# Kernel tuning notes

Hardware: AMD Instinct MI355X
Metric: run time of the kernel (lower is better)

The kernel has to match this reference:

```python
import jax, jax.numpy as jnp
import numpy as np

UNITS = [100, 80, 50, 30]
D_IN = 64


def _lstm_layer(x, Wx, Wh, b):
    # x: [B, T, D]; Wx: [D, 4u]; Wh: [u, 4u]; b: [4u]
    B = x.shape[0]
    u = Wh.shape[0]
    # precompute input contribution for all timesteps: [B, T, 4u]
    xg = jnp.einsum('btd,dg->btg', x, Wx) + b

    def step(carry, xg_t):
        h, c = carry
        g = xg_t + h @ Wh                      # [B, 4u]
        i, f, cbar, o = jnp.split(g, 4, axis=-1)
        i = jax.nn.sigmoid(i)
        f = jax.nn.sigmoid(f)
        o = jax.nn.sigmoid(o)
        c = f * c + i * jnp.tanh(cbar)
        h = o * jnp.tanh(c)
        return (h, c), h

    init = (jnp.zeros((B, u), x.dtype), jnp.zeros((B, u), x.dtype))
    (h_final, _), hs = jax.lax.scan(step, init, jnp.swapaxes(xg, 0, 1))
    return jnp.swapaxes(hs, 0, 1), h_final  # [B, T, u], [B, u]


def setup_inputs() -> dict:
    key = jax.random.key(0)
    ks = jax.random.split(key, 16)
    B, T = 256, 1024
    inp = {"sequence": jax.random.normal(ks[0], (B, T, D_IN), dtype=jnp.float32)}
    d_in = D_IN
    for li, u in enumerate(UNITS):
        s_x = 1.0 / np.sqrt(d_in)
        s_h = 1.0 / np.sqrt(u)
        inp[f"Wx{li}"] = jax.random.normal(ks[1 + 3 * li], (d_in, 4 * u), dtype=jnp.float32) * s_x
        inp[f"Wh{li}"] = jax.random.normal(ks[2 + 3 * li], (u, 4 * u), dtype=jnp.float32) * s_h
        inp[f"b{li}"] = jnp.zeros((4 * u,), dtype=jnp.float32)
        d_in = u
    inp["W_out"] = jax.random.normal(ks[13], (UNITS[-1], 1), dtype=jnp.float32) / np.sqrt(UNITS[-1])
    inp["b_out"] = jnp.zeros((1,), dtype=jnp.float32)
    return inp


def reference(sequence, Wx0, Wh0, b0, Wx1, Wh1, b1, Wx2, Wh2, b2, Wx3, Wh3, b3, W_out, b_out):
    # 4 stacked LSTM layers; dropout is identity at inference.
    x, _ = _lstm_layer(sequence, Wx0, Wh0, b0)   # [B, T, 100]
    x, _ = _lstm_layer(x, Wx1, Wh1, b1)          # [B, T, 80]
    x, _ = _lstm_layer(x, Wx2, Wh2, b2)          # [B, T, 50]
    _, h = _lstm_layer(x, Wx3, Wh3, b3)          # final state [B, 30]
    return h @ W_out + b_out                     # [B, 1]
```

## Files before the change

### kernel.cpp

```cpp
#include <hip/hip_runtime.h>


#define BATCH 256
#define TFULL 1024
#define TC    64
#define NCHUNK (TFULL / TC)
#define NDIAG  (NCHUNK + 3)

typedef __attribute__((ext_vector_type(2))) _Float16 f16x2;
typedef __attribute__((ext_vector_type(4))) _Float16 f16x4;

__device__ __forceinline__ float fast_rcp(float x) {
    return __builtin_amdgcn_rcpf(x);
}

__device__ __forceinline__ float tanh_fast(float x) {
    float e = __expf(-2.0f * fabsf(x));
    float r = fast_rcp(1.0f + e);
    return copysignf(fmaf(2.0f, r, -1.0f), x);
}

__device__ __forceinline__ float fdot2_(f16x2 a, f16x2 b, float c) {
#if __has_builtin(__builtin_amdgcn_fdot2)
    return __builtin_amdgcn_fdot2(a, b, c, false);
#else
    float d;
    asm("v_dot2_f32_f16 %0, %1, %2, %3" : "=v"(d) : "v"(a), "v"(b), "v"(c));
    return d;
#endif
}

__device__ __forceinline__ void lds_barrier() {
    asm volatile("s_waitcnt lgkmcnt(0)\n\ts_barrier" ::: "memory");
}

template<int CTRL>
__device__ __forceinline__ float dpp_add(float v) {
    int t = __builtin_amdgcn_update_dpp(0, __float_as_int(v), CTRL, 0xF, 0xF, true);
    return v + __int_as_float(t);
}
template<int CTRL>
__device__ __forceinline__ float dpp_mov(float v) {
    int t = __builtin_amdgcn_update_dpp(0, __float_as_int(v), CTRL, 0xF, 0xF, true);
    return __int_as_float(t);
}

template<int K, int N>
__device__ __forceinline__ void gemm_body(
    const float* __restrict__ x, int batchStride,
    const float* __restrict__ Wx,
    const float* __restrict__ bias,
    float* __restrict__ out,
    int lid, float* __restrict__ smem)
{
    constexpr int K4   = (K + 3) / 4;
    constexpr int SLAB = 64 * 4 + 4;
    constexpr int GX   = (N + 63) / 64;

    float* s_A = smem;
    float* s_B = smem + K4 * SLAB;

    const int n0   = (lid % GX) * 64;
    const int row0 = (lid / GX) * 64;
    const int tid  = threadIdx.x;
    const int tx   = tid & 15;
    const int ty   = tid >> 4;

    if constexpr ((K % 4) == 0) {
        for (int i = tid; i < 64 * (K / 4); i += 256) {
            const int row = i / (K / 4);
            const int k4  = i % (K / 4);
            const int gr  = row0 + row;
            const int b   = gr >> 6;
            const int t   = gr & 63;
            float4 v = *(const float4*)(x + (size_t)b * batchStride + t * K + k4 * 4);
            *(float4*)(s_A + k4 * SLAB + row * 4) = v;
        }
    } else {
        for (int i = tid; i < 64 * K; i += 256) {
            const int row = i / K;
            const int k   = i % K;
            const int gr  = row0 + row;
            const int b   = gr >> 6;
            const int t   = gr & 63;
            s_A[(k >> 2) * SLAB + row * 4 + (k & 3)] =
                x[(size_t)b * batchStride + t * K + k];
        }
        constexpr int PAD = K4 * 4 - K;
        for (int i = tid; i < 64 * PAD; i += 256) {
            const int row = i / PAD;
            const int kk  = K + i % PAD;
            s_A[(kk >> 2) * SLAB + row * 4 + (kk & 3)] = 0.0f;
        }
    }

    for (int i = tid; i < K4 * 4 * 16; i += 256) {
        const int k  = i >> 4;
        const int c4 = i & 15;
        float4 v = {0.0f, 0.0f, 0.0f, 0.0f};
        if (k < K && n0 + c4 * 4 < N)
            v = *(const float4*)(Wx + (size_t)k * N + n0 + c4 * 4);
        *(float4*)(s_B + k * 64 + c4 * 4) = v;
    }
    __syncthreads();

    float acc[4][4];
#pragma unroll
    for (int r = 0; r < 4; ++r)
#pragma unroll
        for (int c = 0; c < 4; ++c) acc[r][c] = 0.0f;

    for (int k4 = 0; k4 < K4; ++k4) {
        float4 bv[4];
#pragma unroll
        for (int j = 0; j < 4; ++j)
            bv[j] = *(const float4*)(s_B + (k4 * 4 + j) * 64 + tx * 4);
#pragma unroll
        for (int r = 0; r < 4; ++r) {
            float4 av = *(const float4*)(s_A + k4 * SLAB + (ty + 16 * r) * 4);
#pragma unroll
            for (int c = 0; c < 4; ++c) {
                acc[r][c] = fmaf(av.x, ((const float*)&bv[0])[c], acc[r][c]);
                acc[r][c] = fmaf(av.y, ((const float*)&bv[1])[c], acc[r][c]);
                acc[r][c] = fmaf(av.z, ((const float*)&bv[2])[c], acc[r][c]);
                acc[r][c] = fmaf(av.w, ((const float*)&bv[3])[c], acc[r][c]);
            }
        }
    }

    if (n0 + tx * 4 < N) {
        float4 bb = *(const float4*)(bias + n0 + tx * 4);
#pragma unroll
        for (int r = 0; r < 4; ++r) {
            float4 o;
            o.x = acc[r][0] + bb.x;
            o.y = acc[r][1] + bb.y;
            o.z = acc[r][2] + bb.z;
            o.w = acc[r][3] + bb.w;
            *(float4*)(out + (size_t)(row0 + ty + 16 * r) * N + n0 + tx * 4) = o;
        }
    }
}

struct GemmArgs {
    const float *x0, *x1, *x2, *x3;
    float *o0, *o1, *o2, *o3;
    const float *Wx0, *bi0, *Wx1, *bi1, *Wx2, *bi2, *Wx3, *bi3;
    int off1, off2, off3;
};

__global__ __launch_bounds__(256, 2)
void xg_all(GemmArgs a)
{
    __shared__ __align__(16) float smem[12900];
    const int bid = blockIdx.x;
    if (bid < a.off1)
        gemm_body<64, 400>(a.x0, TFULL * 64, a.Wx0, a.bi0, a.o0, bid, smem);
    else if (bid < a.off2)
        gemm_body<100, 320>(a.x1, TC * 100, a.Wx1, a.bi1, a.o1, bid - a.off1, smem);
    else if (bid < a.off3)
        gemm_body<80, 200>(a.x2, TC * 80, a.Wx2, a.bi2, a.o2, bid - a.off2, smem);
    else
        gemm_body<50, 120>(a.x3, TC * 50, a.Wx3, a.bi3, a.o3, bid - a.off3, smem);
}

template<int U, int S, int BLOCK, bool LAST>
__device__ __forceinline__ void rec4_body(
    _Float16* __restrict__ s_h,
    const float* __restrict__ xg,
    const float* __restrict__ Wh,
    float* __restrict__ xout,
    float* __restrict__ c_state,
    float* __restrict__ h_state,
    int first, int b,
    const float* __restrict__ Wout,
    const float* __restrict__ bout,
    float* __restrict__ dout)
{
    constexpr int G  = 4 * U;
    constexpr int HS = 4 * S;

    const int tid = threadIdx.x;
    const int u   = tid >> 2;
    const int s   = tid & 3;
    const bool act_th = (u < U);
    const int uu  = act_th ? u : 0;
    const bool wave_act = ((tid & ~63) < 4 * U);

    f16x2 w4[4][S / 2];
#pragma unroll
    for (int g = 0; g < 4; ++g)
#pragma unroll
        for (int kk = 0; kk < S; kk += 2) {
            const int k0 = s * S + kk;
            const int k1 = k0 + 1;
            const float wa = (act_th && k0 < U) ? Wh[(size_t)k0 * G + g * U + uu] : 0.0f;
            const float wb = (act_th && k1 < U) ? Wh[(size_t)k1 * G + g * U + uu] : 0.0f;
            w4[g][kk >> 1] = (f16x2){(_Float16)wa, (_Float16)wb};
        }

    for (int i = tid; i < 2 * HS; i += BLOCK) s_h[i] = (_Float16)0.0f;
    __syncthreads();
    if (tid < U) s_h[tid] = (_Float16)(first ? 0.0f : h_state[b * U + tid]);
    float c = first ? 0.0f : c_state[b * U + uu];
    __syncthreads();

    const float* xgp = xg + (size_t)b * TC * G + (s * U + uu);
    float xg0 = xgp[0];
    float xg1 = xgp[G];

    int cur = 0;
    float h = 0.0f, hprev = 0.0f;
    const bool is_t = (s == 2);

    for (int t = 0; t < TC; ++t, cur ^= 1) {
        if (wave_act) {
            const int tp = (t + 2 < TC) ? (t + 2) : (TC - 1);
            const float xg2 = xgp[(size_t)tp * G];

            if (!LAST) {
                if (act_th && s == 0 && t > 0)
                    xout[((size_t)b * TC + (t - 1)) * U + u] = hprev;
            }

            float a0 = 0.0f, a1 = 0.0f, a2 = 0.0f, a3 = 0.0f;
            const _Float16* hs = s_h + cur * HS + s * S;
#pragma unroll
            for (int kk = 0; kk < S; kk += 4) {
                f16x4 v = *(const f16x4*)(hs + kk);
                f16x2 lo = __builtin_shufflevector(v, v, 0, 1);
                f16x2 hi = __builtin_shufflevector(v, v, 2, 3);
                const int p = kk >> 1;
                a0 = fdot2_(lo, w4[0][p],     a0);
                a0 = fdot2_(hi, w4[0][p + 1], a0);
                a1 = fdot2_(lo, w4[1][p],     a1);
                a1 = fdot2_(hi, w4[1][p + 1], a1);
                a2 = fdot2_(lo, w4[2][p],     a2);
                a2 = fdot2_(hi, w4[2][p + 1], a2);
                a3 = fdot2_(lo, w4[3][p],     a3);
                a3 = fdot2_(hi, w4[3][p + 1], a3);
            }

            a0 = dpp_add<0xB1>(a0); a0 = dpp_add<0x4E>(a0);
            a1 = dpp_add<0xB1>(a1); a1 = dpp_add<0x4E>(a1);
            a2 = dpp_add<0xB1>(a2); a2 = dpp_add<0x4E>(a2);
            a3 = dpp_add<0xB1>(a3); a3 = dpp_add<0x4E>(a3);

            const float asum = (s == 0) ? a0 : (s == 1) ? a1 : (s == 2) ? a2 : a3;
            const float gs = asum + xg0;
            const float y  = is_t ? (-2.0f * fabsf(gs)) : (-gs);
            const float r  = fast_rcp(1.0f + __expf(y));
            const float v  = is_t ? copysignf(fmaf(2.0f, r, -1.0f), gs) : r;

            const float fi = dpp_mov<0x00>(v);
            const float ff = dpp_mov<0x55>(v);
            const float tc = dpp_mov<0xAA>(v);
            const float fo = dpp_mov<0xFF>(v);
            c = fmaf(ff, c, fi * tc);
            h = fo * tanh_fast(c);

            const int nxt = cur ^ 1;
            if (act_th && s == 0) s_h[nxt * HS + u] = (_Float16)h;
            hprev = h;
            xg0 = xg1; xg1 = xg2;
        }
        lds_barrier();
    }

    if (!LAST) {
        if (act_th && s == 0)
            xout[((size_t)b * TC + (TC - 1)) * U + u] = hprev;
    }
    if (act_th && s == 0) {
        c_state[b * U + u] = c;
        h_state[b * U + u] = h;
    }
    if (LAST && tid == 0) {
        float acc = bout[0];
#pragma unroll
        for (int k = 0; k < U; ++k)
            acc = fmaf((float)s_h[cur * HS + k], Wout[k], acc);
        dout[b] = acc;
    }
}

struct RecArgs {
    const float *xg0, *xg1, *xg2, *xg3;
    const float *Wh0, *Wh1, *Wh2, *Wh3;
    float *xc0, *xc1, *xc2;
    float *c0, *h0, *c1, *h1, *c2, *h2, *c3, *h3;
    const float *Wout, *bout;
    float *dout;
    int d;
};

__global__ __attribute__((amdgpu_flat_work_group_size(448, 448),
                          amdgpu_waves_per_eu(4, 8)))
void rec_all(RecArgs a)
{
    __shared__ __align__(16) _Float16 s_h[2 * 112];
    const int grp = blockIdx.x >> 8;
    const int b   = blockIdx.x & 255;
    const int j   = a.d - grp;
    if (j < 0 || j >= NCHUNK) return;
    const int first = (j == 0) ? 1 : 0;
    switch (grp) {
    case 0: rec4_body<100, 28, 448, false>(s_h, a.xg0, a.Wh0, a.xc0, a.c0, a.h0,
                                           first, b, nullptr, nullptr, nullptr); break;
    case 1: rec4_body< 80, 20, 448, false>(s_h, a.xg1, a.Wh1, a.xc1, a.c1, a.h1,
                                           first, b, nullptr, nullptr, nullptr); break;
    case 2: rec4_body< 50, 16, 448, false>(s_h, a.xg2, a.Wh2, a.xc2, a.c2, a.h2,
                                           first, b, nullptr, nullptr, nullptr); break;
    default: rec4_body< 30,  8, 448, true >(s_h, a.xg3, a.Wh3, nullptr, a.c3, a.h3,
                                           first, b, a.Wout, a.bout, a.dout); break;
    }
}

extern "C" void kernel_launch(void* const* d_in, const int* in_sizes, int n_in,
                              void* d_out, int out_size, void* d_ws, size_t ws_size,
                              hipStream_t stream)
{
    const float* seq  = (const float*)d_in[0];
    const float* Wx0  = (const float*)d_in[1];
    const float* Wh0  = (const float*)d_in[2];
    const float* b0   = (const float*)d_in[3];
    const float* Wx1  = (const float*)d_in[4];
    const float* Wh1  = (const float*)d_in[5];
    const float* b1   = (const float*)d_in[6];
    const float* Wx2  = (const float*)d_in[7];
    const float* Wh2  = (const float*)d_in[8];
    const float* b2   = (const float*)d_in[9];
    const float* Wx3  = (const float*)d_in[10];
    const float* Wh3  = (const float*)d_in[11];
    const float* b3   = (const float*)d_in[12];
    const float* Wout = (const float*)d_in[13];
    const float* bout = (const float*)d_in[14];
    float* out = (float*)d_out;

    float* ws  = (float*)d_ws;
    float* XG0 = ws;
    float* XG1 = XG0 + (size_t)BATCH * TC * 400;
    float* XG2 = XG1 + (size_t)BATCH * TC * 320;
    float* XG3 = XG2 + (size_t)BATCH * TC * 200;
    float* XC0 = XG3 + (size_t)BATCH * TC * 120;
    float* XC1 = XC0 + (size_t)BATCH * TC * 100;
    float* XC2 = XC1 + (size_t)BATCH * TC * 80;
    float* st  = XC2 + (size_t)BATCH * TC * 50;
    float* sc0 = st + 0 * 32768; float* sh0 = st + 1 * 32768;
    float* sc1 = st + 2 * 32768; float* sh1 = st + 3 * 32768;
    float* sc2 = st + 4 * 32768; float* sh2 = st + 5 * 32768;
    float* sc3 = st + 6 * 32768; float* sh3 = st + 7 * 32768;

    const int NB0 = 7 * 256, NB1 = 5 * 256, NB2 = 4 * 256, NB3 = 2 * 256;

    for (int d = 0; d < NDIAG; ++d) {
        GemmArgs ga;
        ga.x0 = nullptr; ga.x1 = nullptr; ga.x2 = nullptr; ga.x3 = nullptr;
        ga.o0 = XG0; ga.o1 = XG1; ga.o2 = XG2; ga.o3 = XG3;
        ga.Wx0 = Wx0; ga.bi0 = b0; ga.Wx1 = Wx1; ga.bi1 = b1;
        ga.Wx2 = Wx2; ga.bi2 = b2; ga.Wx3 = Wx3; ga.bi3 = b3;
        int nb = 0;
        if (d < NCHUNK)                { ga.x0 = seq + (size_t)d * TC * 64; nb += NB0; }
        ga.off1 = nb;
        if (d >= 1 && d - 1 < NCHUNK)  { ga.x1 = XC0; nb += NB1; }
        ga.off2 = nb;
        if (d >= 2 && d - 2 < NCHUNK)  { ga.x2 = XC1; nb += NB2; }
        ga.off3 = nb;
        if (d >= 3 && d - 3 < NCHUNK)  { ga.x3 = XC2; nb += NB3; }

        xg_all<<<dim3(nb), dim3(256), 0, stream>>>(ga);

        RecArgs ra;
        ra.xg0 = XG0; ra.xg1 = XG1; ra.xg2 = XG2; ra.xg3 = XG3;
        ra.Wh0 = Wh0; ra.Wh1 = Wh1; ra.Wh2 = Wh2; ra.Wh3 = Wh3;
        ra.xc0 = XC0; ra.xc1 = XC1; ra.xc2 = XC2;
        ra.c0 = sc0; ra.h0 = sh0; ra.c1 = sc1; ra.h1 = sh1;
        ra.c2 = sc2; ra.h2 = sh2; ra.c3 = sc3; ra.h3 = sh3;
        ra.Wout = Wout; ra.bout = bout; ra.dout = out;
        ra.d = d;

        rec_all<<<dim3(4 * 256), dim3(448), 0, stream>>>(ra);
    }
}
```

Baseline: 3.086 ms.

## Split each hidden unit's recurrence across two lanes instead of four

Restructures the recurrent kernel so each hidden unit is handled by 2 lanes instead of 4. Each lane now computes half of the K-dimension dot product for all four gates and evaluates two gate nonlinearities. The block shrinks from 448 to 256 threads, and the reductions and gate exchanges need fewer DPP steps. In exchange, each lane does twice as many fdot2 operations and holds twice as many weight registers; waves_per_eu is pinned to 1.

```diff
diff --git a/kernel.cpp b/kernel.cpp
--- a/kernel.cpp
+++ b/kernel.cpp
@@ -165,7 +165,7 @@
 }
 
 template<int U, int S, int BLOCK, bool LAST>
-__device__ __forceinline__ void rec4_body(
+__device__ __forceinline__ void rec2_body(
     _Float16* __restrict__ s_h,
     const float* __restrict__ xg,
     const float* __restrict__ Wh,
@@ -178,25 +178,25 @@
     float* __restrict__ dout)
 {
     constexpr int G  = 4 * U;
-    constexpr int HS = 4 * S;
+    constexpr int HS = 2 * S;
 
     const int tid = threadIdx.x;
-    const int u   = tid >> 2;
-    const int s   = tid & 3;
+    const int u   = tid >> 1;
+    const int s   = tid & 1;
     const bool act_th = (u < U);
     const int uu  = act_th ? u : 0;
-    const bool wave_act = ((tid & ~63) < 4 * U);
-
-    f16x2 w4[4][S / 2];
+    const bool wave_act = ((tid & ~63) < 2 * U);
+
+    f16x2 w[4][S / 2];
 #pragma unroll
     for (int g = 0; g < 4; ++g)
 #pragma unroll
-        for (int kk = 0; kk < S; kk += 2) {
-            const int k0 = s * S + kk;
+        for (int p = 0; p < S / 2; ++p) {
+            const int k0 = s * S + 2 * p;
             const int k1 = k0 + 1;
             const float wa = (act_th && k0 < U) ? Wh[(size_t)k0 * G + g * U + uu] : 0.0f;
             const float wb = (act_th && k1 < U) ? Wh[(size_t)k1 * G + g * U + uu] : 0.0f;
-            w4[g][kk >> 1] = (f16x2){(_Float16)wa, (_Float16)wb};
+            w[g][p] = (f16x2){(_Float16)wa, (_Float16)wb};
         }
 
     for (int i = tid; i < 2 * HS; i += BLOCK) s_h[i] = (_Float16)0.0f;
@@ -205,18 +205,20 @@
     float c = first ? 0.0f : c_state[b * U + uu];
     __syncthreads();
 
-    const float* xgp = xg + (size_t)b * TC * G + (s * U + uu);
-    float xg0 = xgp[0];
-    float xg1 = xgp[G];
+    const float* xgpA = xg + (size_t)b * TC * G + (s * U + uu);
+    const float* xgpB = xgpA + 2 * U;
+    float xA0 = xgpA[0], xA1 = xgpA[G];
+    float xB0 = xgpB[0], xB1 = xgpB[G];
 
     int cur = 0;
     float h = 0.0f, hprev = 0.0f;
-    const bool is_t = (s == 2);
+    const bool is_t = (s == 0);
 
     for (int t = 0; t < TC; ++t, cur ^= 1) {
         if (wave_act) {
             const int tp = (t + 2 < TC) ? (t + 2) : (TC - 1);
-            const float xg2 = xgp[(size_t)tp * G];
+            const float xA2 = xgpA[(size_t)tp * G];
+            const float xB2 = xgpB[(size_t)tp * G];
 
             if (!LAST) {
                 if (act_th && s == 0 && t > 0)
@@ -231,38 +233,42 @@
                 f16x2 lo = __builtin_shufflevector(v, v, 0, 1);
                 f16x2 hi = __builtin_shufflevector(v, v, 2, 3);
                 const int p = kk >> 1;
-                a0 = fdot2_(lo, w4[0][p],     a0);
-                a0 = fdot2_(hi, w4[0][p + 1], a0);
-                a1 = fdot2_(lo, w4[1][p],     a1);
-                a1 = fdot2_(hi, w4[1][p + 1], a1);
-                a2 = fdot2_(lo, w4[2][p],     a2);
-                a2 = fdot2_(hi, w4[2][p + 1], a2);
-                a3 = fdot2_(lo, w4[3][p],     a3);
-                a3 = fdot2_(hi, w4[3][p + 1], a3);
+                a0 = fdot2_(lo, w[0][p],     a0);
+                a0 = fdot2_(hi, w[0][p + 1], a0);
+                a1 = fdot2_(lo, w[1][p],     a1);
+                a1 = fdot2_(hi, w[1][p + 1], a1);
+                a2 = fdot2_(lo, w[2][p],     a2);
+                a2 = fdot2_(hi, w[2][p + 1], a2);
+                a3 = fdot2_(lo, w[3][p],     a3);
+                a3 = fdot2_(hi, w[3][p + 1], a3);
             }
 
-            a0 = dpp_add<0xB1>(a0); a0 = dpp_add<0x4E>(a0);
-            a1 = dpp_add<0xB1>(a1); a1 = dpp_add<0x4E>(a1);
-            a2 = dpp_add<0xB1>(a2); a2 = dpp_add<0x4E>(a2);
-            a3 = dpp_add<0xB1>(a3); a3 = dpp_add<0x4E>(a3);
-
-            const float asum = (s == 0) ? a0 : (s == 1) ? a1 : (s == 2) ? a2 : a3;
-            const float gs = asum + xg0;
-            const float y  = is_t ? (-2.0f * fabsf(gs)) : (-gs);
-            const float r  = fast_rcp(1.0f + __expf(y));
-            const float v  = is_t ? copysignf(fmaf(2.0f, r, -1.0f), gs) : r;
-
-            const float fi = dpp_mov<0x00>(v);
-            const float ff = dpp_mov<0x55>(v);
-            const float tc = dpp_mov<0xAA>(v);
-            const float fo = dpp_mov<0xFF>(v);
+            a0 = dpp_add<0xB1>(a0);
+            a1 = dpp_add<0xB1>(a1);
+            a2 = dpp_add<0xB1>(a2);
+            a3 = dpp_add<0xB1>(a3);
+
+            const float gA = ((s == 0) ? a0 : a1) + xA0;
+            const float gB = ((s == 0) ? a2 : a3) + xB0;
+            const float rA = fast_rcp(1.0f + __expf(-gA));
+            const float yB = is_t ? (-2.0f * fabsf(gB)) : (-gB);
+            const float rB = fast_rcp(1.0f + __expf(yB));
+            const float vB = is_t ? copysignf(fmaf(2.0f, rB, -1.0f), gB) : rB;
+
+            const float Asw = dpp_mov<0xB1>(rA);
+            const float Bsw = dpp_mov<0xB1>(vB);
+            const float fi = (s == 0) ? rA  : Asw;
+            const float ff = (s == 0) ? Asw : rA;
+            const float tc = (s == 0) ? vB  : Bsw;
+            const float fo = (s == 0) ? Bsw : vB;
             c = fmaf(ff, c, fi * tc);
             h = fo * tanh_fast(c);
 
             const int nxt = cur ^ 1;
             if (act_th && s == 0) s_h[nxt * HS + u] = (_Float16)h;
             hprev = h;
-            xg0 = xg1; xg1 = xg2;
+            xA0 = xA1; xA1 = xA2;
+            xB0 = xB1; xB1 = xB2;
         }
         lds_barrier();
     }
@@ -294,24 +300,24 @@
     int d;
 };
 
-__global__ __attribute__((amdgpu_flat_work_group_size(448, 448),
-                          amdgpu_waves_per_eu(4, 8)))
+__global__ __attribute__((amdgpu_flat_work_group_size(256, 256),
+                          amdgpu_waves_per_eu(1, 1)))
 void rec_all(RecArgs a)
 {
-    __shared__ __align__(16) _Float16 s_h[2 * 112];
+    __shared__ __align__(16) _Float16 s_h[2 * 104];
     const int grp = blockIdx.x >> 8;
     const int b   = blockIdx.x & 255;
     const int j   = a.d - grp;
     if (j < 0 || j >= NCHUNK) return;
     const int first = (j == 0) ? 1 : 0;
     switch (grp) {
-    case 0: rec4_body<100, 28, 448, false>(s_h, a.xg0, a.Wh0, a.xc0, a.c0, a.h0,
+    case 0: rec2_body<100, 52, 256, false>(s_h, a.xg0, a.Wh0, a.xc0, a.c0, a.h0,
                                            first, b, nullptr, nullptr, nullptr); break;
-    case 1: rec4_body< 80, 20, 448, false>(s_h, a.xg1, a.Wh1, a.xc1, a.c1, a.h1,
+    case 1: rec2_body< 80, 40, 256, false>(s_h, a.xg1, a.Wh1, a.xc1, a.c1, a.h1,
                                            first, b, nullptr, nullptr, nullptr); break;
-    case 2: rec4_body< 50, 16, 448, false>(s_h, a.xg2, a.Wh2, a.xc2, a.c2, a.h2,
+    case 2: rec2_body< 50, 28, 256, false>(s_h, a.xg2, a.Wh2, a.xc2, a.c2, a.h2,
                                            first, b, nullptr, nullptr, nullptr); break;
-    default: rec4_body< 30,  8, 448, true >(s_h, a.xg3, a.Wh3, nullptr, a.c3, a.h3,
+    default: rec2_body< 30, 16, 256, true >(s_h, a.xg3, a.Wh3, nullptr, a.c3, a.h3,
                                            first, b, a.Wout, a.bout, a.dout); break;
     }
 }
@@ -379,6 +385,6 @@
         ra.Wout = Wout; ra.bout = bout; ra.dout = out;
         ra.d = d;
 
-        rec_all<<<dim3(4 * 256), dim3(448), 0, stream>>>(ra);
-    }
-}
+        rec_all<<<dim3(4 * 256), dim3(256), 0, stream>>>(ra);
+    }
+}
```

Measured after the change: 5.164 ms. 1.67x slower.
